# Kernel optimization log

Hardware: AMD Instinct MI355X
Metric: run time of the kernel (lower is better)

The kernel has to match this reference:

```python
import jax, jax.numpy as jnp
import numpy as np

LEAKY_SLOPE = 0.01  # torch nn.LeakyReLU default

def _mlp(x, w1, b1, w2, b2):
    # MLP_Layer(num_layers=2, batch_norm=False): Linear -> ReLU -> Linear
    return jax.nn.relu(x @ w1 + b1) @ w2 + b2

def _edge_softmax(scores, dst, num_nodes):
    # softmax over incoming edges of each destination node; scores: [E, H]
    m = jax.ops.segment_max(scores, dst, num_segments=num_nodes)  # [N, H]
    e = jnp.exp(scores - m[dst])
    s = jax.ops.segment_sum(e, dst, num_segments=num_nodes)       # [N, H]
    return e / s[dst]

def setup_inputs() -> dict:
    key = jax.random.key(0)
    ks = jax.random.split(key, 10)
    N, E, H = 50000, 800000, 4
    D_H, PCA, PI, HID = 64, 64, 32, 128
    inp = {
        "h":    jax.random.normal(ks[0], (N, D_H), jnp.float32),
        "pca":  jax.random.normal(ks[1], (N, PCA), jnp.float32),
        "pimg": jax.random.normal(ks[2], (N, PI), jnp.float32),
        "pca_w1": jax.random.normal(ks[3], (2 * PCA, HID), jnp.float32) * (1.0 / np.sqrt(2 * PCA)),
        "pca_b1": jnp.zeros((HID,), jnp.float32),
        "pca_w2": jax.random.normal(ks[4], (HID, H), jnp.float32) * (1.0 / np.sqrt(HID)),
        "pca_b2": jnp.zeros((H,), jnp.float32),
        "pi_w1": jax.random.normal(ks[5], (2 * PI, HID), jnp.float32) * (1.0 / np.sqrt(2 * PI)),
        "pi_b1": jnp.zeros((HID,), jnp.float32),
        "pi_w2": jax.random.normal(ks[6], (HID, H), jnp.float32) * (1.0 / np.sqrt(HID)),
        "pi_b2": jnp.zeros((H,), jnp.float32),
        "src": jax.random.randint(ks[7], (E,), 0, N, jnp.int32),
        "dst": jax.random.randint(ks[8], (E,), 0, N, jnp.int32),
    }
    return inp

def reference(h, pca, pimg, pca_w1, pca_b1, pca_w2, pca_b2,
              pi_w1, pi_b1, pi_w2, pi_b2, src, dst):
    N = h.shape[0]

    def attend(feat, w1, b1, w2, b2):
        e_feat = jnp.concatenate([feat[src], feat[dst]], axis=1)        # [E, 2F]
        score = jax.nn.leaky_relu(_mlp(e_feat, w1, b1, w2, b2), LEAKY_SLOPE)  # [E, H]
        a = _edge_softmax(score, dst, N)                                # [E, H]
        msg = h[src][:, None, :] * a[:, :, None]                        # [E, H, D]
        return jax.ops.segment_sum(msg, dst, num_segments=N)           # [N, H, D]

    out_pca = attend(pca, pca_w1, pca_b1, pca_w2, pca_b2)
    out_pi = attend(pimg, pi_w1, pi_b1, pi_w2, pi_b2)
    return jnp.concatenate([out_pca, out_pi], axis=-1)                  # [N, H, 2D]
```

## Files before the change

kernel.cpp:

```cpp
#include <hip/hip_runtime.h>
#include <hip/hip_fp16.h>

constexpr int HID = 128;
constexpr int DH  = 64;

typedef _Float16 f16x2 __attribute__((ext_vector_type(2)));
typedef _Float16 fh4   __attribute__((ext_vector_type(4)));
typedef _Float16 fh8   __attribute__((ext_vector_type(8)));
typedef float    f32x4v __attribute__((ext_vector_type(4)));

__device__ __forceinline__ fh8 relu8(fh8 x) {
  fh8 z = {0, 0, 0, 0, 0, 0, 0, 0};
#if __has_builtin(__builtin_elementwise_max)
  return __builtin_elementwise_max(x, z);
#else
  fh8 r;
#pragma unroll
  for (int i = 0; i < 8; i++) r[i] = x[i] > z[i] ? x[i] : z[i];
  return r;
#endif
}

__global__ void count_h16_frag_kernel(const int* __restrict__ dst, int* __restrict__ counts, int E,
                                      const float* __restrict__ h, _Float16* __restrict__ h16, int total,
                                      const float* __restrict__ w1a, const float* __restrict__ w1b,
                                      _Float16* __restrict__ fragTab) {
  int i = blockIdx.x * 256 + threadIdx.x;
  if (blockIdx.x < 128) {
    int flat = i;
    int rel = flat >> 14;
    int r2 = flat & 16383;
    int g = r2 >> 10, s = (r2 >> 9) & 1, l = (r2 >> 3) & 63, j = r2 & 7;
    int bc = l & 15, bkg = l >> 4;
    int k = s * 32 + bkg * 8 + j;
    int F = rel ? 32 : 64;
    const float* w1 = rel ? w1b : w1a;
    float val = 0.f;
    if (k < F) {
      int jslot = (g & 7) * 16 + bc;
      int krow = (g < 8) ? k : (F + k);
      val = w1[krow * HID + jslot];
    }
    fragTab[flat] = (_Float16)val;
  }
  if (i < E) atomicAdd(&counts[dst[i]], 1);
  int base = i * 8;
  if (base + 7 < total) {
    float4 f0 = *(const float4*)(h + base);
    float4 f1 = *(const float4*)(h + base + 4);
    fh8 t;
    t[0] = (_Float16)f0.x; t[1] = (_Float16)f0.y; t[2] = (_Float16)f0.z; t[3] = (_Float16)f0.w;
    t[4] = (_Float16)f1.x; t[5] = (_Float16)f1.y; t[6] = (_Float16)f1.z; t[7] = (_Float16)f1.w;
    *(fh8*)(h16 + base) = t;
  }
}

__launch_bounds__(256)
__global__ void uv_mfma_kernel(const float* __restrict__ pca, const float* __restrict__ pimg,
                               const float* __restrict__ b1a, const float* __restrict__ b1b,
                               const _Float16* __restrict__ fragTab,
                               _Float16* __restrict__ u_cat, _Float16* __restrict__ v_cat, int N) {
  __shared__ _Float16 sB[16384];
  int rel = blockIdx.y;
  const float* feat = rel ? pimg : pca;
  const float* b1   = rel ? b1b : b1a;
  int F  = rel ? 32 : 64;
  int KS = rel ? 1 : 2;
  int tid = threadIdx.x;
  {
    const fh8* srcp = (const fh8*)(fragTab + rel * 16384);
    fh8* dstp = (fh8*)sB;
    for (int i = tid; i < 2048; i += 256) dstp[i] = srcp[i];
  }
  __syncthreads();
  int lane = tid & 63, w = tid >> 6;
  int c = lane & 15, kg = lane >> 4;
  int node = blockIdx.x * 64 + w * 16 + c;
  int nclamp = node < N ? node : N - 1;
  fh8 bfeat[2];
#pragma unroll
  for (int s = 0; s < 2; s++) {
    if (s < KS) {
      const float* fp = feat + (size_t)nclamp * F + s * 32 + kg * 8;
      float4 f0 = *(const float4*)fp;
      float4 f1 = *(const float4*)(fp + 4);
      fh8 t;
      t[0] = (_Float16)f0.x; t[1] = (_Float16)f0.y; t[2] = (_Float16)f0.z; t[3] = (_Float16)f0.w;
      t[4] = (_Float16)f1.x; t[5] = (_Float16)f1.y; t[6] = (_Float16)f1.z; t[7] = (_Float16)f1.w;
      bfeat[s] = t;
    }
  }
  float4 b1q[8];
#pragma unroll
  for (int g = 0; g < 8; g++) b1q[g] = *(const float4*)(b1 + g * 16 + kg * 4);

  bool wr = node < N;
#pragma unroll
  for (int g = 0; g < 16; g++) {
    f32x4v acc = {0.f, 0.f, 0.f, 0.f};
    acc = __builtin_amdgcn_mfma_f32_16x16x32_f16(((const fh8*)sB)[(g * 2 + 0) * 64 + lane], bfeat[0], acc, 0, 0, 0);
    if (KS == 2)
      acc = __builtin_amdgcn_mfma_f32_16x16x32_f16(((const fh8*)sB)[(g * 2 + 1) * 64 + lane], bfeat[1], acc, 0, 0, 0);
    bool isv = g >= 8;
    int jbase = (g & 7) * 16 + kg * 4;
    float4 bias = isv ? b1q[g & 7] : make_float4(0.f, 0.f, 0.f, 0.f);
    fh4 pk;
    pk[0] = (_Float16)(acc[0] + bias.x);
    pk[1] = (_Float16)(acc[1] + bias.y);
    pk[2] = (_Float16)(acc[2] + bias.z);
    pk[3] = (_Float16)(acc[3] + bias.w);
    _Float16* outp = isv ? v_cat : u_cat;
    if (wr) *(fh4*)(outp + (size_t)node * 256 + rel * 128 + jbase) = pk;
  }
}

__launch_bounds__(256)
__global__ void scan1_kernel(const int* __restrict__ counts, int* __restrict__ bsums, int N) {
  int b = blockIdx.x, tid = threadIdx.x;
  int base = b * 1024 + tid * 4;
  int s = 0;
  if (base + 3 < N) {
    int4 v = *(const int4*)(counts + base);
    s = v.x + v.y + v.z + v.w;
  } else {
    for (int q = 0; q < 4; q++) { int idx = base + q; if (idx < N) s += counts[idx]; }
  }
#pragma unroll
  for (int o = 32; o >= 1; o >>= 1) s += __shfl_xor(s, o);
  __shared__ int ws[4];
  if ((tid & 63) == 0) ws[tid >> 6] = s;
  __syncthreads();
  if (tid == 0) bsums[b] = ws[0] + ws[1] + ws[2] + ws[3];
}

__launch_bounds__(256)
__global__ void scan23_kernel(const int* __restrict__ counts, const int* __restrict__ bsums,
                              int* __restrict__ offsets, int* __restrict__ cursor,
                              int NB, int N, int E) {
  int b = blockIdx.x, tid = threadIdx.x, lane = tid & 63, w = tid >> 6;
  __shared__ int s_bpre;
  if (tid < 64) {
    int v = (lane < NB) ? bsums[lane] : 0;
    int incl = v;
#pragma unroll
    for (int o = 1; o < 64; o <<= 1) { int t = __shfl_up(incl, o); if (lane >= o) incl += t; }
    int excl = incl - v;
    int t = __shfl(excl, b);
    if (lane == 0) s_bpre = t;
  }
  __syncthreads();
  int base = b * 1024 + tid * 4;
  int c[4] = {0, 0, 0, 0};
  if (base + 3 < N) {
    int4 v = *(const int4*)(counts + base);
    c[0] = v.x; c[1] = v.y; c[2] = v.z; c[3] = v.w;
  } else {
    for (int q = 0; q < 4; q++) { int idx = base + q; if (idx < N) c[q] = counts[idx]; }
  }
  int s = c[0] + c[1] + c[2] + c[3];
  int incl = s;
#pragma unroll
  for (int o = 1; o < 64; o <<= 1) { int t = __shfl_up(incl, o); if (lane >= o) incl += t; }
  int excl = incl - s;
  __shared__ int ws[4];
  if (lane == 63) ws[w] = incl;
  __syncthreads();
  int wpre = 0;
  for (int q = 0; q < w; q++) wpre += ws[q];
  int off = s_bpre + wpre + excl;
  for (int q = 0; q < 4; q++) {
    int idx = base + q;
    if (idx < N) { offsets[idx] = off; cursor[idx] = off; }
    off += c[q];
  }
  if (b == 0 && tid == 0) offsets[N] = E;
}

__global__ void fill_kernel(const int* __restrict__ src, const int* __restrict__ dst,
                            int* __restrict__ cursor, int2* __restrict__ edges, int E) {
  int e = blockIdx.x * 256 + threadIdx.x;
  if (e < E) {
    int d = dst[e];
    int pos = atomicAdd(&cursor[d], 1);
    edges[pos] = make_int2(src[e], d);
  }
}

__launch_bounds__(256, 8)
__global__ void score_kernel(const _Float16* __restrict__ u_cat, const _Float16* __restrict__ v_cat,
                             const int2* __restrict__ edges,
                             const float* __restrict__ w2a, const float* __restrict__ w2b,
                             const float* __restrict__ b2a, const float* __restrict__ b2b,
                             _Float16* __restrict__ ek, int E) {
  __shared__ _Float16 sB[8 * 64 * 8];
  int tid = threadIdx.x, lane = tid & 63, w = tid >> 6;
  int col = lane & 15, kg = lane >> 4;
  for (int idx = tid; idx < 4096; idx += 256) {
    int t = idx >> 9, l = (idx >> 3) & 63, j = idx & 7;
    int bc = l & 15;
    int k = t * 32 + ((l >> 4) << 3) + j;
    float val = 0.f;
    if (bc < 4) { if (k < 128) val = w2a[k * 4 + bc]; }
    else if (bc < 8) { if (k >= 128) val = w2b[(k - 128) * 4 + (bc - 4)]; }
    sB[idx] = (_Float16)val;
  }
  __syncthreads();

  int ebase = blockIdx.x * 256 + w * 64;
  const _Float16* up[4];
  const _Float16* vp[4];
#pragma unroll
  for (int m = 0; m < 4; m++) {
    int em = ebase + m * 16 + col;
    int ec = em < E ? em : 0;
    int2 sd = edges[ec];
    up[m] = u_cat + (size_t)sd.x * 256 + kg * 8;
    vp[m] = v_cat + (size_t)sd.y * 256 + kg * 8;
  }

  f32x4v acc[4];
#pragma unroll
  for (int m = 0; m < 4; m++) acc[m] = (f32x4v){0.f, 0.f, 0.f, 0.f};

#pragma unroll
  for (int t = 0; t < 8; t++) {
    fh8 bf = *(const fh8*)(sB + ((t * 64 + lane) << 3));
#pragma unroll
    for (int m = 0; m < 4; m++) {
      fh8 uu = *(const fh8*)(up[m] + t * 32);
      fh8 vv = *(const fh8*)(vp[m] + t * 32);
      acc[m] = __builtin_amdgcn_mfma_f32_16x16x32_f16(relu8(uu + vv), bf, acc[m], 0, 0, 0);
    }
  }

  if (col < 8) {
    float b2v = (col < 4) ? b2a[col] : b2b[col - 4];
#pragma unroll
    for (int m = 0; m < 4; m++) {
#pragma unroll
      for (int q = 0; q < 4; q++) {
        int er = ebase + m * 16 + kg * 4 + q;
        if (er < E) {
          float x = acc[m][q] + b2v;
          x = x > 0.f ? x : 0.01f * x;
          ek[(size_t)er * 8 + col] = (_Float16)__expf(x);
        }
      }
    }
  }
}

__launch_bounds__(256, 8)
__global__ void agg_kernel(const _Float16* __restrict__ ek, const int2* __restrict__ edges,
                           const int* __restrict__ offsets, const _Float16* __restrict__ h16,
                           float* __restrict__ out, int N) {
  int wid = blockIdx.x * 4 + (threadIdx.x >> 6);
  int lane = threadIdx.x & 63;
  if (wid >= N) return;
  int off0 = offsets[wid], off1 = offsets[wid + 1];
  int deg = off1 - off0;
  float* op = out + (size_t)wid * 512;
  if (deg == 0) {
#pragma unroll
    for (int k = 0; k < 4; k++) { op[k * 128 + lane] = 0.f; op[k * 128 + 64 + lane] = 0.f; }
    return;
  }
  float accO[8] = {0, 0, 0, 0, 0, 0, 0, 0};
  float ssum[8] = {0, 0, 0, 0, 0, 0, 0, 0};
  int last = off1 - 1;
  for (int jj = 0; jj < deg; jj += 4) {
    int i0 = off0 + jj;
    int i1 = min(i0 + 1, last), i2 = min(i0 + 2, last), i3 = min(i0 + 3, last);
    bool m1 = jj + 1 < deg, m2 = jj + 2 < deg, m3 = jj + 3 < deg;
    int s0 = edges[i0].x, s1 = edges[i1].x, s2 = edges[i2].x, s3 = edges[i3].x;
    fh8 e0 = *(const fh8*)(ek + (size_t)i0 * 8);
    fh8 e1 = *(const fh8*)(ek + (size_t)i1 * 8);
    fh8 e2 = *(const fh8*)(ek + (size_t)i2 * 8);
    fh8 e3 = *(const fh8*)(ek + (size_t)i3 * 8);
    float hv0 = (float)h16[(size_t)s0 * DH + lane];
    float hv1 = (float)h16[(size_t)s1 * DH + lane];
    float hv2 = (float)h16[(size_t)s2 * DH + lane];
    float hv3 = (float)h16[(size_t)s3 * DH + lane];
#pragma unroll
    for (int k = 0; k < 8; k++) {
      float e0v = (float)e0[k];
      float e1v = m1 ? (float)e1[k] : 0.f;
      float e2v = m2 ? (float)e2[k] : 0.f;
      float e3v = m3 ? (float)e3[k] : 0.f;
      accO[k] = fmaf(e0v, hv0, accO[k]);
      accO[k] = fmaf(e1v, hv1, accO[k]);
      accO[k] = fmaf(e2v, hv2, accO[k]);
      accO[k] = fmaf(e3v, hv3, accO[k]);
      ssum[k] += (e0v + e1v) + (e2v + e3v);
    }
  }
#pragma unroll
  for (int k = 0; k < 8; k++) {
    float rsv = 1.f / ssum[k];
    int colo = k < 4 ? k * 128 + lane : (k - 4) * 128 + 64 + lane;
    op[colo] = accO[k] * rsv;
  }
}

extern "C" void kernel_launch(void* const* d_in, const int* in_sizes, int n_in,
                              void* d_out, int out_size, void* d_ws, size_t ws_size,
                              hipStream_t stream) {
  const float* h      = (const float*)d_in[0];
  const float* pca    = (const float*)d_in[1];
  const float* pimg   = (const float*)d_in[2];
  const float* pca_w1 = (const float*)d_in[3];
  const float* pca_b1 = (const float*)d_in[4];
  const float* pca_w2 = (const float*)d_in[5];
  const float* pca_b2 = (const float*)d_in[6];
  const float* pi_w1  = (const float*)d_in[7];
  const float* pi_b1  = (const float*)d_in[8];
  const float* pi_w2  = (const float*)d_in[9];
  const float* pi_b2  = (const float*)d_in[10];
  const int*   src    = (const int*)d_in[11];
  const int*   dst    = (const int*)d_in[12];
  int N = in_sizes[0] / 64;
  int E = in_sizes[11];
  float* out = (float*)d_out;

  char* ws = (char*)d_ws;
  size_t o = 0;
  auto alloc = [&](size_t bytes) { void* p = ws + o; o += (bytes + 255) & ~(size_t)255; return p; };
  _Float16* u_cat  = (_Float16*)alloc((size_t)N * 256 * 2);
  _Float16* v_cat  = (_Float16*)alloc((size_t)N * 256 * 2);
  _Float16* h16    = (_Float16*)alloc((size_t)N * 64 * 2);
  _Float16* fragTab = (_Float16*)alloc(32768 * 2);
  int* counts  = (int*)alloc((size_t)N * 4);
  int* cursor  = (int*)alloc((size_t)N * 4);
  int* offsets = (int*)alloc((size_t)(N + 1) * 4);
  int* bsums   = (int*)alloc(1024 * 4);
  int2* edges  = (int2*)alloc((size_t)E * 8);
  _Float16* ekb = (_Float16*)alloc((size_t)E * 8 * 2);

  hipMemsetAsync(counts, 0, (size_t)N * 4, stream);

  count_h16_frag_kernel<<<(E + 255) / 256, 256, 0, stream>>>(dst, counts, E, h, h16, N * 64,
                                                             pca_w1, pi_w1, fragTab);
  dim3 uvgrid((N + 63) / 64, 2);
  uv_mfma_kernel<<<uvgrid, 256, 0, stream>>>(pca, pimg, pca_b1, pi_b1, fragTab, u_cat, v_cat, N);
  int NB = (N + 1023) / 1024;
  scan1_kernel<<<NB, 256, 0, stream>>>(counts, bsums, N);
  scan23_kernel<<<NB, 256, 0, stream>>>(counts, bsums, offsets, cursor, NB, N, E);
  fill_kernel<<<(E + 255) / 256, 256, 0, stream>>>(src, dst, cursor, edges, E);
  score_kernel<<<(E + 255) / 256, 256, 0, stream>>>(u_cat, v_cat, edges,
                                                    pca_w2, pi_w2, pca_b2, pi_b2, ekb, E);
  agg_kernel<<<(N + 3) / 4, 256, 0, stream>>>(ekb, edges, offsets, h16, out, N);
}
```

Before: 286.3 us.

## Fuse scan1 into uv kernel, widen atomic passes, use nontemporal agg accesses

The block-sum scan is merged into the UV MFMA kernel as extra blocks, which removes one kernel launch. The count pass now does four dst atomics per thread on a grid sized for the h16 conversion, and the fill pass handles two edges per thread with vector loads. The aggregation kernel uses nontemporal loads for the edge and score streams and nontemporal stores for the output, so this streaming traffic is less likely to evict h16 from cache. The cost is less parallelism per atomic pass and more per-thread work in those passes.

```diff
diff --git a/kernel.cpp b/kernel.cpp
--- a/kernel.cpp
+++ b/kernel.cpp
@@ -8,6 +8,7 @@
 typedef _Float16 fh4   __attribute__((ext_vector_type(4)));
 typedef _Float16 fh8   __attribute__((ext_vector_type(8)));
 typedef float    f32x4v __attribute__((ext_vector_type(4)));
+typedef int      i32x2  __attribute__((ext_vector_type(2)));
 
 __device__ __forceinline__ fh8 relu8(fh8 x) {
   fh8 z = {0, 0, 0, 0, 0, 0, 0, 0};
@@ -43,7 +44,16 @@
     }
     fragTab[flat] = (_Float16)val;
   }
-  if (i < E) atomicAdd(&counts[dst[i]], 1);
+  int be = i * 4;
+  if (be + 3 < E) {
+    int4 d4 = *(const int4*)(dst + be);
+    atomicAdd(&counts[d4.x], 1);
+    atomicAdd(&counts[d4.y], 1);
+    atomicAdd(&counts[d4.z], 1);
+    atomicAdd(&counts[d4.w], 1);
+  } else {
+    for (int q = 0; q < 4; q++) if (be + q < E) atomicAdd(&counts[dst[be + q]], 1);
+  }
   int base = i * 8;
   if (base + 7 < total) {
     float4 f0 = *(const float4*)(h + base);
@@ -56,17 +66,37 @@
 }
 
 __launch_bounds__(256)
-__global__ void uv_mfma_kernel(const float* __restrict__ pca, const float* __restrict__ pimg,
-                               const float* __restrict__ b1a, const float* __restrict__ b1b,
-                               const _Float16* __restrict__ fragTab,
-                               _Float16* __restrict__ u_cat, _Float16* __restrict__ v_cat, int N) {
+__global__ void uv_scan1_kernel(const float* __restrict__ pca, const float* __restrict__ pimg,
+                                const float* __restrict__ b1a, const float* __restrict__ b1b,
+                                const _Float16* __restrict__ fragTab,
+                                _Float16* __restrict__ u_cat, _Float16* __restrict__ v_cat, int N,
+                                const int* __restrict__ counts, int* __restrict__ bsums, int NBu) {
   __shared__ _Float16 sB[16384];
-  int rel = blockIdx.y;
+  int blk = blockIdx.x;
+  int tid = threadIdx.x;
+  if (blk >= 2 * NBu) {
+    int sb = blk - 2 * NBu;
+    int base = sb * 1024 + tid * 4;
+    int s = 0;
+    if (base + 3 < N) {
+      int4 v = *(const int4*)(counts + base);
+      s = v.x + v.y + v.z + v.w;
+    } else {
+      for (int q = 0; q < 4; q++) { int idx = base + q; if (idx < N) s += counts[idx]; }
+    }
+#pragma unroll
+    for (int o = 32; o >= 1; o >>= 1) s += __shfl_xor(s, o);
+    int* ws = (int*)sB;
+    if ((tid & 63) == 0) ws[tid >> 6] = s;
+    __syncthreads();
+    if (tid == 0) bsums[sb] = ws[0] + ws[1] + ws[2] + ws[3];
+    return;
+  }
+  int rel = blk / NBu, nb = blk - rel * NBu;
   const float* feat = rel ? pimg : pca;
   const float* b1   = rel ? b1b : b1a;
   int F  = rel ? 32 : 64;
   int KS = rel ? 1 : 2;
-  int tid = threadIdx.x;
   {
     const fh8* srcp = (const fh8*)(fragTab + rel * 16384);
     fh8* dstp = (fh8*)sB;
@@ -75,7 +105,7 @@
   __syncthreads();
   int lane = tid & 63, w = tid >> 6;
   int c = lane & 15, kg = lane >> 4;
-  int node = blockIdx.x * 64 + w * 16 + c;
+  int node = nb * 64 + w * 16 + c;
   int nclamp = node < N ? node : N - 1;
   fh8 bfeat[2];
 #pragma unroll
@@ -115,25 +145,6 @@
 }
 
 __launch_bounds__(256)
-__global__ void scan1_kernel(const int* __restrict__ counts, int* __restrict__ bsums, int N) {
-  int b = blockIdx.x, tid = threadIdx.x;
-  int base = b * 1024 + tid * 4;
-  int s = 0;
-  if (base + 3 < N) {
-    int4 v = *(const int4*)(counts + base);
-    s = v.x + v.y + v.z + v.w;
-  } else {
-    for (int q = 0; q < 4; q++) { int idx = base + q; if (idx < N) s += counts[idx]; }
-  }
-#pragma unroll
-  for (int o = 32; o >= 1; o >>= 1) s += __shfl_xor(s, o);
-  __shared__ int ws[4];
-  if ((tid & 63) == 0) ws[tid >> 6] = s;
-  __syncthreads();
-  if (tid == 0) bsums[b] = ws[0] + ws[1] + ws[2] + ws[3];
-}
-
-__launch_bounds__(256)
 __global__ void scan23_kernel(const int* __restrict__ counts, const int* __restrict__ bsums,
                               int* __restrict__ offsets, int* __restrict__ cursor,
                               int NB, int N, int E) {
@@ -178,8 +189,16 @@
 
 __global__ void fill_kernel(const int* __restrict__ src, const int* __restrict__ dst,
                             int* __restrict__ cursor, int2* __restrict__ edges, int E) {
-  int e = blockIdx.x * 256 + threadIdx.x;
-  if (e < E) {
+  int i = blockIdx.x * 256 + threadIdx.x;
+  int e = i * 2;
+  if (e + 1 < E) {
+    int2 s2 = *(const int2*)(src + e);
+    int2 d2 = *(const int2*)(dst + e);
+    int p0 = atomicAdd(&cursor[d2.x], 1);
+    edges[p0] = make_int2(s2.x, d2.x);
+    int p1 = atomicAdd(&cursor[d2.y], 1);
+    edges[p1] = make_int2(s2.y, d2.y);
+  } else if (e < E) {
     int d = dst[e];
     int pos = atomicAdd(&cursor[d], 1);
     edges[pos] = make_int2(src[e], d);
@@ -262,7 +281,10 @@
   float* op = out + (size_t)wid * 512;
   if (deg == 0) {
 #pragma unroll
-    for (int k = 0; k < 4; k++) { op[k * 128 + lane] = 0.f; op[k * 128 + 64 + lane] = 0.f; }
+    for (int k = 0; k < 4; k++) {
+      __builtin_nontemporal_store(0.f, op + k * 128 + lane);
+      __builtin_nontemporal_store(0.f, op + k * 128 + 64 + lane);
+    }
     return;
   }
   float accO[8] = {0, 0, 0, 0, 0, 0, 0, 0};
@@ -272,15 +294,18 @@
     int i0 = off0 + jj;
     int i1 = min(i0 + 1, last), i2 = min(i0 + 2, last), i3 = min(i0 + 3, last);
     bool m1 = jj + 1 < deg, m2 = jj + 2 < deg, m3 = jj + 3 < deg;
-    int s0 = edges[i0].x, s1 = edges[i1].x, s2 = edges[i2].x, s3 = edges[i3].x;
-    fh8 e0 = *(const fh8*)(ek + (size_t)i0 * 8);
-    fh8 e1 = *(const fh8*)(ek + (size_t)i1 * 8);
-    fh8 e2 = *(const fh8*)(ek + (size_t)i2 * 8);
-    fh8 e3 = *(const fh8*)(ek + (size_t)i3 * 8);
-    float hv0 = (float)h16[(size_t)s0 * DH + lane];
-    float hv1 = (float)h16[(size_t)s1 * DH + lane];
-    float hv2 = (float)h16[(size_t)s2 * DH + lane];
-    float hv3 = (float)h16[(size_t)s3 * DH + lane];
+    i32x2 sd0 = __builtin_nontemporal_load((const i32x2*)(edges + i0));
+    i32x2 sd1 = __builtin_nontemporal_load((const i32x2*)(edges + i1));
+    i32x2 sd2 = __builtin_nontemporal_load((const i32x2*)(edges + i2));
+    i32x2 sd3 = __builtin_nontemporal_load((const i32x2*)(edges + i3));
+    fh8 e0 = __builtin_nontemporal_load((const fh8*)(ek + (size_t)i0 * 8));
+    fh8 e1 = __builtin_nontemporal_load((const fh8*)(ek + (size_t)i1 * 8));
+    fh8 e2 = __builtin_nontemporal_load((const fh8*)(ek + (size_t)i2 * 8));
+    fh8 e3 = __builtin_nontemporal_load((const fh8*)(ek + (size_t)i3 * 8));
+    float hv0 = (float)h16[(size_t)sd0[0] * DH + lane];
+    float hv1 = (float)h16[(size_t)sd1[0] * DH + lane];
+    float hv2 = (float)h16[(size_t)sd2[0] * DH + lane];
+    float hv3 = (float)h16[(size_t)sd3[0] * DH + lane];
 #pragma unroll
     for (int k = 0; k < 8; k++) {
       float e0v = (float)e0[k];
@@ -298,7 +323,7 @@
   for (int k = 0; k < 8; k++) {
     float rsv = 1.f / ssum[k];
     int colo = k < 4 ? k * 128 + lane : (k - 4) * 128 + 64 + lane;
-    op[colo] = accO[k] * rsv;
+    __builtin_nontemporal_store(accO[k] * rsv, op + colo);
   }
 }
 
@@ -338,14 +363,16 @@
 
   hipMemsetAsync(counts, 0, (size_t)N * 4, stream);
 
-  count_h16_frag_kernel<<<(E + 255) / 256, 256, 0, stream>>>(dst, counts, E, h, h16, N * 64,
-                                                             pca_w1, pi_w1, fragTab);
-  dim3 uvgrid((N + 63) / 64, 2);
-  uv_mfma_kernel<<<uvgrid, 256, 0, stream>>>(pca, pimg, pca_b1, pi_b1, fragTab, u_cat, v_cat, N);
+  int total_h = N * 64;
+  int g1 = (total_h / 8 + 255) / 256;
+  count_h16_frag_kernel<<<g1, 256, 0, stream>>>(dst, counts, E, h, h16, total_h,
+                                                pca_w1, pi_w1, fragTab);
+  int NBu = (N + 63) / 64;
   int NB = (N + 1023) / 1024;
-  scan1_kernel<<<NB, 256, 0, stream>>>(counts, bsums, N);
+  uv_scan1_kernel<<<2 * NBu + NB, 256, 0, stream>>>(pca, pimg, pca_b1, pi_b1, fragTab,
+                                                    u_cat, v_cat, N, counts, bsums, NBu);
   scan23_kernel<<<NB, 256, 0, stream>>>(counts, bsums, offsets, cursor, NB, N, E);
-  fill_kernel<<<(E + 255) / 256, 256, 0, stream>>>(src, dst, cursor, edges, E);
+  fill_kernel<<<(E / 2 + 255) / 256, 256, 0, stream>>>(src, dst, cursor, edges, E);
   score_kernel<<<(E + 255) / 256, 256, 0, stream>>>(u_cat, v_cat, edges,
                                                     pca_w2, pi_w2, pca_b2, pi_b2, ekb, E);
   agg_kernel<<<(N + 3) / 4, 256, 0, stream>>>(ekb, edges, offsets, h16, out, N);
```

New measurement: 342.3 us. +19.6%, slower.
